# Performance work log

Measured on AMD Instinct MI355X. Metric: run time of the kernel, lower is better.

Reference implementation:

```python
import jax, jax.numpy as jnp
import numpy as np

N_GRAPHS = 512
N_PER_G = 84
N = N_GRAPHS * N_PER_G            # 43008 nodes
E = N_GRAPHS * N_PER_G * N_PER_G  # 3612672 edges (fully connected incl. self-loops)


def setup_inputs() -> dict:
    key = jax.random.key(0)
    ks = jax.random.split(key, 10)
    x = jax.random.normal(ks[0], (N, 84), dtype=jnp.float32)
    # fully-connected edge_index per graph: [2, E], row0=src j, row1=dst i
    off = (np.arange(N_GRAPHS) * N_PER_G)[:, None, None]
    src = (off + np.arange(N_PER_G)[:, None]) + np.zeros((1, 1, N_PER_G), np.int64)
    dst = (off + np.arange(N_PER_G)[None, None, :]) + np.zeros((1, N_PER_G, 1), np.int64)
    edge_index = jnp.asarray(np.stack([src.reshape(-1), dst.reshape(-1)]), dtype=jnp.int64)
    batch = jnp.asarray(np.repeat(np.arange(N_GRAPHS), N_PER_G), dtype=jnp.int64)
    s = 0.1
    W1 = jax.random.normal(ks[1], (84, 64), dtype=jnp.float32) * s
    a_src1 = jax.random.normal(ks[2], (32, 2), dtype=jnp.float32) * s
    a_dst1 = jax.random.normal(ks[3], (32, 2), dtype=jnp.float32) * s
    b1 = jnp.zeros((64,), jnp.float32)
    W2 = jax.random.normal(ks[4], (64, 64), dtype=jnp.float32) * s
    a_src2 = jax.random.normal(ks[5], (1, 64), dtype=jnp.float32) * s
    a_dst2 = jax.random.normal(ks[6], (1, 64), dtype=jnp.float32) * s
    b2 = jnp.zeros((64,), jnp.float32)
    Wfc = jax.random.normal(ks[7], (64, 1), dtype=jnp.float32) * s
    bfc = jnp.zeros((1,), jnp.float32)
    return {"x": x, "edge_index": edge_index, "batch": batch,
            "W1": W1, "a_src1": a_src1, "a_dst1": a_dst1, "b1": b1,
            "W2": W2, "a_src2": a_src2, "a_dst2": a_dst2, "b2": b2,
            "Wfc": Wfc, "bfc": bfc}


def gat_conv(x, W, a_src, a_dst, bias, src, dst, n_heads, ch):
    # x: [N, F] -> h: [N, H, C]
    h = (x @ W).reshape(-1, n_heads, ch)
    alpha_src = jnp.sum(h * a_src, axis=-1)  # [N, H]
    alpha_dst = jnp.sum(h * a_dst, axis=-1)  # [N, H]
    e = jax.nn.leaky_relu(alpha_src[src] + alpha_dst[dst], 0.2)  # [E, H]
    # segment softmax over edges grouped by destination node
    m = jax.ops.segment_max(e, dst, num_segments=N)
    e = jnp.exp(e - m[dst])
    z = jax.ops.segment_sum(e, dst, num_segments=N)
    alpha = e / (z[dst] + 1e-16)                              # [E, H]
    msg = h[src] * alpha[:, :, None]                          # [E, H, C]
    out = jax.ops.segment_sum(msg, dst, num_segments=N)       # [N, H, C]
    return out.reshape(-1, n_heads * ch) + bias


def reference(x, edge_index, batch, W1, a_src1, a_dst1, b1, W2, a_src2, a_dst2, b2, Wfc, bfc):
    src, dst = edge_index[0], edge_index[1]
    h = gat_conv(x, W1, a_src1, a_dst1, b1, src, dst, 32, 2)   # [N, 64]
    h = jax.nn.elu(h)
    h = gat_conv(h, W2, a_src2, a_dst2, b2, src, dst, 1, 64)   # [N, 64]
    # global mean pool per graph
    sums = jax.ops.segment_sum(h, batch, num_segments=N_GRAPHS)
    cnts = jax.ops.segment_sum(jnp.ones((N, 1), h.dtype), batch, num_segments=N_GRAPHS)
    pooled = sums / cnts                                       # [B, 64]
    out = pooled @ Wfc + bfc                                   # [B, 1]
    z = jnp.zeros((1,), jnp.float32)
    return (out, z, z, z, z, z, z)
```

## Files before the change

### kernel.cpp

```cpp
#include <hip/hip_runtime.h>

#define NG 512
#define P  84
#define F0 84
#define F1 64
#define L2E 1.4426950408889634f

#if __has_builtin(__builtin_amdgcn_exp2f)
#define EXP2F(v) __builtin_amdgcn_exp2f(v)
#else
#define EXP2F(v) exp2f(v)
#endif
#if __has_builtin(__builtin_amdgcn_rcpf)
#define RCPF(v) __builtin_amdgcn_rcpf(v)
#else
#define RCPF(v) (1.0f / (v))
#endif


__launch_bounds__(256, 2)
__global__ void gat_fused(const float* __restrict__ x,
                          const float* __restrict__ W1,
                          const float* __restrict__ a_src1,
                          const float* __restrict__ a_dst1,
                          const float* __restrict__ b1,
                          const float* __restrict__ W2,
                          const float* __restrict__ a_src2,
                          const float* __restrict__ a_dst2,
                          const float* __restrict__ b2,
                          const float* __restrict__ Wfc,
                          const float* __restrict__ bfc,
                          float* __restrict__ out)
{
  __shared__ float xs[P * F0];
  __shared__ float wbuf[P * F1];
  __shared__ float h1s[P * F1];
  __shared__ float a2s[2 * F1];
  __shared__ float2 as2p[P];
  __shared__ float2 ad2p[P];
  __shared__ float reds[4 * P];
  __shared__ float redt[P];

  const int tid = threadIdx.x;
  const int ln  = tid & 63;
  const int wid = tid >> 6;
  const int g   = blockIdx.x;
  const int i0  = wid * 21;

  if (g == 0 && tid < 6) out[NG + tid] = 0.f;

  {
    const float4* w4 = (const float4*)W1;
    float4* s4 = (float4*)wbuf;
    #pragma unroll
    for (int t = 0; t < 6; ++t) {
      int idx = tid + t * 256;
      if (idx < (P * F1) / 4) s4[idx] = w4[idx];
    }
    const float4* x4 = (const float4*)(x + (size_t)g * P * F0);
    float4* xs4 = (float4*)xs;
    #pragma unroll
    for (int t = 0; t < 7; ++t) {
      int idx = tid + t * 256;
      if (idx < (P * F0) / 4) xs4[idx] = x4[idx];
    }
    if (tid < F1) a2s[tid] = a_src2[tid] * L2E;
    else if (tid < 2 * F1) a2s[tid] = a_dst2[tid - F1] * L2E;
  }
  __syncthreads();

  {
    float wk[44];
    #pragma unroll
    for (int k = 0; k < 44; ++k) wk[k] = wbuf[k * F1 + ln];
    #pragma unroll 2
    for (int ii = 0; ii < 21; ++ii) {
      const float4* rp = (const float4*)&xs[(i0 + ii) * F0];
      float c0 = 0.f, c1 = 0.f, c2 = 0.f, c3 = 0.f;
      #pragma unroll
      for (int kq = 0; kq < 11; ++kq) {
        float4 v = rp[kq];
        c0 = fmaf(v.x, wk[4 * kq + 0], c0);
        c1 = fmaf(v.y, wk[4 * kq + 1], c1);
        c2 = fmaf(v.z, wk[4 * kq + 2], c2);
        c3 = fmaf(v.w, wk[4 * kq + 3], c3);
      }
      h1s[(i0 + ii) * F1 + ln] = (c0 + c1) + (c2 + c3);
    }
  }
  {
    float wk[40];
    #pragma unroll
    for (int k = 0; k < 40; ++k) wk[k] = wbuf[(44 + k) * F1 + ln];
    #pragma unroll 2
    for (int ii = 0; ii < 21; ++ii) {
      const float4* rp = (const float4*)&xs[(i0 + ii) * F0];
      float c0 = h1s[(i0 + ii) * F1 + ln], c1 = 0.f, c2 = 0.f, c3 = 0.f;
      #pragma unroll
      for (int kq = 0; kq < 10; ++kq) {
        float4 v = rp[11 + kq];
        c0 = fmaf(v.x, wk[4 * kq + 0], c0);
        c1 = fmaf(v.y, wk[4 * kq + 1], c1);
        c2 = fmaf(v.z, wk[4 * kq + 2], c2);
        c3 = fmaf(v.w, wk[4 * kq + 3], c3);
      }
      h1s[(i0 + ii) * F1 + ln] = (c0 + c1) + (c2 + c3);
    }
  }
  __syncthreads();

  {
    float2* pq = (float2*)xs;
    #pragma unroll
    for (int r = 0; r < 11; ++r) {
      int idx = tid + r * 256;
      if (idx < P * 32) {
        int j = idx >> 5, h = idx & 31;
        float2 c = *(const float2*)&h1s[j * F1 + 2 * h];
        float asj = fmaf(c.x, a_src1[2 * h] * L2E, c.y * (a_src1[2 * h + 1] * L2E));
        float2 e; e.x = EXP2F(asj); e.y = EXP2F(0.2f * asj);
        pq[idx] = e;
      }
    }
  }
  const float4* w24 = (const float4*)W2;
  float4 w2r0 = w24[tid];
  float4 w2r1 = w24[tid + 256];
  float4 w2r2 = w24[tid + 512];
  float4 w2r3 = w24[tid + 768];
  __syncthreads();

  {
    const int h  = tid & 31;
    const int ig = tid >> 5;
    const float ada = a_dst1[2 * h] * L2E, adb = a_dst1[2 * h + 1] * L2E;
    float pi[11], qi[11], sm[11], m0[11], m1[11];
    #pragma unroll
    for (int t = 0; t < 11; ++t) {
      int i = ig + 8 * t; int ie = i < P ? i : P - 1;
      float2 c = *(const float2*)&h1s[ie * F1 + 2 * h];
      float adi = fmaf(c.x, ada, c.y * adb);
      pi[t] = EXP2F(adi); qi[t] = EXP2F(0.2f * adi);
      sm[t] = 0.f; m0[t] = 0.f; m1[t] = 0.f;
    }
    const float2* pq = (const float2*)xs;
    #pragma unroll 2
    for (int j = 0; j < P; ++j) {
      float2 c = *(const float2*)&h1s[j * F1 + 2 * h];
      float2 e = pq[j * 32 + h];
      #pragma unroll
      for (int t = 0; t < 11; ++t) {
        float p = fmaxf(e.x * pi[t], e.y * qi[t]);
        sm[t] += p;
        m0[t] = fmaf(p, c.x, m0[t]);
        m1[t] = fmaf(p, c.y, m1[t]);
      }
    }
    const float bc0 = b1[2 * h], bc1 = b1[2 * h + 1];
    float* o1 = wbuf;
    #pragma unroll
    for (int t = 0; t < 11; ++t) {
      int i = ig + 8 * t;
      if (i < P) {
        float rz = RCPF(sm[t]);
        float u0 = fmaf(m0[t], rz, bc0);
        float u1 = fmaf(m1[t], rz, bc1);
        u0 = u0 > 0.f ? u0 : (__expf(u0) - 1.f);
        u1 = u1 > 0.f ? u1 : (__expf(u1) - 1.f);
        float2 oo; oo.x = u0; oo.y = u1;
        *(float2*)&o1[i * F1 + 2 * h] = oo;
      }
    }
  }
  __syncthreads();

  {
    float4* s4 = (float4*)xs;
    s4[tid]       = w2r0;
    s4[tid + 256] = w2r1;
    s4[tid + 512] = w2r2;
    s4[tid + 768] = w2r3;
  }
  __syncthreads();

  {
    float wk[32];
    #pragma unroll
    for (int k = 0; k < 32; ++k) wk[k] = xs[k * F1 + ln];
    #pragma unroll 2
    for (int ii = 0; ii < 21; ++ii) {
      const float4* rp = (const float4*)&wbuf[(i0 + ii) * F1];
      float c0 = 0.f, c1 = 0.f, c2 = 0.f, c3 = 0.f;
      #pragma unroll
      for (int kq = 0; kq < 8; ++kq) {
        float4 v = rp[kq];
        c0 = fmaf(v.x, wk[4 * kq + 0], c0);
        c1 = fmaf(v.y, wk[4 * kq + 1], c1);
        c2 = fmaf(v.z, wk[4 * kq + 2], c2);
        c3 = fmaf(v.w, wk[4 * kq + 3], c3);
      }
      h1s[(i0 + ii) * F1 + ln] = (c0 + c1) + (c2 + c3);
    }
  }
  {
    float wk[32];
    #pragma unroll
    for (int k = 0; k < 32; ++k) wk[k] = xs[(32 + k) * F1 + ln];
    #pragma unroll 2
    for (int ii = 0; ii < 21; ++ii) {
      const float4* rp = (const float4*)&wbuf[(i0 + ii) * F1];
      float c0 = h1s[(i0 + ii) * F1 + ln], c1 = 0.f, c2 = 0.f, c3 = 0.f;
      #pragma unroll
      for (int kq = 0; kq < 8; ++kq) {
        float4 v = rp[8 + kq];
        c0 = fmaf(v.x, wk[4 * kq + 0], c0);
        c1 = fmaf(v.y, wk[4 * kq + 1], c1);
        c2 = fmaf(v.z, wk[4 * kq + 2], c2);
        c3 = fmaf(v.w, wk[4 * kq + 3], c3);
      }
      h1s[(i0 + ii) * F1 + ln] = (c0 + c1) + (c2 + c3);
    }
  }
  __syncthreads();

  if (tid < P) {
    float s = 0.f, d = 0.f;
    #pragma unroll 4
    for (int f = 0; f < F1; ++f) {
      int fp = (f + tid) & 63;
      float c = h1s[tid * F1 + fp];
      s = fmaf(c, a2s[fp], s);
      d = fmaf(c, a2s[F1 + fp], d);
    }
    float2 ps; ps.x = EXP2F(s); ps.y = EXP2F(0.2f * s);
    float2 pd; pd.x = EXP2F(d); pd.y = EXP2F(0.2f * d);
    as2p[tid] = ps; ad2p[tid] = pd;
  }
  __syncthreads();

  {
    const float2 S0 = as2p[ln];
    float2 S1; S1.x = 0.f; S1.y = 0.f;
    if (ln < P - 64) S1 = as2p[64 + ln];
    float sj0 = 0.f, sj1 = 0.f;
    for (int ii = 0; ii < 21; ++ii) {
      float2 D = ad2p[i0 + ii];
      float p0 = fmaxf(S0.x * D.x, S0.y * D.y);
      float p1 = (ln < P - 64) ? fmaxf(S1.x * D.x, S1.y * D.y) : 0.f;
      float ss = p0 + p1;
      #pragma unroll
      for (int off = 32; off > 0; off >>= 1) ss += __shfl_xor(ss, off, 64);
      float rz = RCPF(ss);
      sj0 = fmaf(p0, rz, sj0);
      sj1 = fmaf(p1, rz, sj1);
    }
    reds[wid * P + ln] = sj0;
    if (ln < P - 64) reds[wid * P + 64 + ln] = sj1;
  }
  __syncthreads();

  if (tid < P) {
    float s = 0.f;
    #pragma unroll
    for (int w = 0; w < 4; ++w) s += reds[w * P + tid];
    redt[tid] = s;
  }
  __syncthreads();

  if (wid == 0) {
    float c0 = 0.f, c1 = 0.f, c2 = 0.f, c3 = 0.f;
    for (int j = 0; j < P; j += 4) {
      c0 = fmaf(redt[j],     h1s[(j + 0) * F1 + ln], c0);
      c1 = fmaf(redt[j + 1], h1s[(j + 1) * F1 + ln], c1);
      c2 = fmaf(redt[j + 2], h1s[(j + 2) * F1 + ln], c2);
      c3 = fmaf(redt[j + 3], h1s[(j + 3) * F1 + ln], c3);
    }
    float pooled = ((c0 + c1) + (c2 + c3)) * (1.f / 84.f) + b2[ln];
    float v = pooled * Wfc[ln];
    #pragma unroll
    for (int off = 32; off > 0; off >>= 1) v += __shfl_xor(v, off, 64);
    if (ln == 0) out[g] = v + bfc[0];
  }
}

extern "C" void kernel_launch(void* const* d_in, const int* in_sizes, int n_in,
                              void* d_out, int out_size, void* d_ws, size_t ws_size,
                              hipStream_t stream) {
  const float* x      = (const float*)d_in[0];
  const float* W1     = (const float*)d_in[3];
  const float* a_src1 = (const float*)d_in[4];
  const float* a_dst1 = (const float*)d_in[5];
  const float* b1     = (const float*)d_in[6];
  const float* W2     = (const float*)d_in[7];
  const float* a_src2 = (const float*)d_in[8];
  const float* a_dst2 = (const float*)d_in[9];
  const float* b2     = (const float*)d_in[10];
  const float* Wfc    = (const float*)d_in[11];
  const float* bfc    = (const float*)d_in[12];
  hipLaunchKernelGGL(gat_fused, dim3(NG), dim3(256), 0, stream,
                     x, W1, a_src1, a_dst1, b1, W2, a_src2, a_dst2, b2, Wfc, bfc,
                     (float*)d_out);
}
```

Measured before the change: 153.5 us.

## Read x rows directly from global, shrink LDS, split attention dot across lanes

Drops the shared-memory staging of the per-graph x tile. The first GEMM now reads x rows straight from global memory using a wave-uniform offset (readfirstlane), so the loads can become scalar or broadcast. The pq/W2 scratch gets its own smaller buffer, cutting LDS usage, which may allow higher occupancy, and W2 is staged with float2 loads. The layer-2 attention-score dot product is split across two lanes per node and combined with a shuffle. The cost is more global-memory traffic in the GEMM, relying on cache hits for the repeated row reads.

```diff
diff --git a/kernel.cpp b/kernel.cpp
--- a/kernel.cpp
+++ b/kernel.cpp
@@ -32,14 +32,14 @@
                           const float* __restrict__ bfc,
                           float* __restrict__ out)
 {
-  __shared__ float xs[P * F0];
-  __shared__ float wbuf[P * F1];
-  __shared__ float h1s[P * F1];
-  __shared__ float a2s[2 * F1];
+  __shared__ float  wbuf[P * F1];
+  __shared__ float  h1s[P * F1];
+  __shared__ float2 pqs[P * 32];
+  __shared__ float  a2s[2 * F1];
   __shared__ float2 as2p[P];
   __shared__ float2 ad2p[P];
-  __shared__ float reds[4 * P];
-  __shared__ float redt[P];
+  __shared__ float  reds[4 * P];
+  __shared__ float  redt[P];
 
   const int tid = threadIdx.x;
   const int ln  = tid & 63;
@@ -49,6 +49,8 @@
 
   if (g == 0 && tid < 6) out[NG + tid] = 0.f;
 
+  const float* xg = x + (size_t)g * P * F0;
+
   {
     const float4* w4 = (const float4*)W1;
     float4* s4 = (float4*)wbuf;
@@ -57,13 +59,6 @@
       int idx = tid + t * 256;
       if (idx < (P * F1) / 4) s4[idx] = w4[idx];
     }
-    const float4* x4 = (const float4*)(x + (size_t)g * P * F0);
-    float4* xs4 = (float4*)xs;
-    #pragma unroll
-    for (int t = 0; t < 7; ++t) {
-      int idx = tid + t * 256;
-      if (idx < (P * F0) / 4) xs4[idx] = x4[idx];
-    }
     if (tid < F1) a2s[tid] = a_src2[tid] * L2E;
     else if (tid < 2 * F1) a2s[tid] = a_dst2[tid - F1] * L2E;
   }
@@ -75,7 +70,8 @@
     for (int k = 0; k < 44; ++k) wk[k] = wbuf[k * F1 + ln];
     #pragma unroll 2
     for (int ii = 0; ii < 21; ++ii) {
-      const float4* rp = (const float4*)&xs[(i0 + ii) * F0];
+      const int roff = __builtin_amdgcn_readfirstlane((i0 + ii) * F0);
+      const float4* rp = (const float4*)(xg + roff);
       float c0 = 0.f, c1 = 0.f, c2 = 0.f, c3 = 0.f;
       #pragma unroll
       for (int kq = 0; kq < 11; ++kq) {
@@ -94,7 +90,8 @@
     for (int k = 0; k < 40; ++k) wk[k] = wbuf[(44 + k) * F1 + ln];
     #pragma unroll 2
     for (int ii = 0; ii < 21; ++ii) {
-      const float4* rp = (const float4*)&xs[(i0 + ii) * F0];
+      const int roff = __builtin_amdgcn_readfirstlane((i0 + ii) * F0);
+      const float4* rp = (const float4*)(xg + roff);
       float c0 = h1s[(i0 + ii) * F1 + ln], c1 = 0.f, c2 = 0.f, c3 = 0.f;
       #pragma unroll
       for (int kq = 0; kq < 10; ++kq) {
@@ -110,7 +107,6 @@
   __syncthreads();
 
   {
-    float2* pq = (float2*)xs;
     #pragma unroll
     for (int r = 0; r < 11; ++r) {
       int idx = tid + r * 256;
@@ -119,15 +115,14 @@
         float2 c = *(const float2*)&h1s[j * F1 + 2 * h];
         float asj = fmaf(c.x, a_src1[2 * h] * L2E, c.y * (a_src1[2 * h + 1] * L2E));
         float2 e; e.x = EXP2F(asj); e.y = EXP2F(0.2f * asj);
-        pq[idx] = e;
-      }
-    }
-  }
-  const float4* w24 = (const float4*)W2;
-  float4 w2r0 = w24[tid];
-  float4 w2r1 = w24[tid + 256];
-  float4 w2r2 = w24[tid + 512];
-  float4 w2r3 = w24[tid + 768];
+        pqs[idx] = e;
+      }
+    }
+  }
+  const float2* w22 = (const float2*)W2;
+  float2 w2r[8];
+  #pragma unroll
+  for (int t = 0; t < 8; ++t) w2r[t] = w22[tid + t * 256];
   __syncthreads();
 
   {
@@ -143,11 +138,10 @@
       pi[t] = EXP2F(adi); qi[t] = EXP2F(0.2f * adi);
       sm[t] = 0.f; m0[t] = 0.f; m1[t] = 0.f;
     }
-    const float2* pq = (const float2*)xs;
     #pragma unroll 2
     for (int j = 0; j < P; ++j) {
       float2 c = *(const float2*)&h1s[j * F1 + 2 * h];
-      float2 e = pq[j * 32 + h];
+      float2 e = pqs[j * 32 + h];
       #pragma unroll
       for (int t = 0; t < 11; ++t) {
         float p = fmaxf(e.x * pi[t], e.y * qi[t]);
@@ -175,18 +169,17 @@
   __syncthreads();
 
   {
-    float4* s4 = (float4*)xs;
-    s4[tid]       = w2r0;
-    s4[tid + 256] = w2r1;
-    s4[tid + 512] = w2r2;
-    s4[tid + 768] = w2r3;
-  }
-  __syncthreads();
-
-  {
+    float2* s2 = (float2*)pqs;
+    #pragma unroll
+    for (int t = 0; t < 8; ++t) s2[tid + t * 256] = w2r[t];
+  }
+  __syncthreads();
+
+  {
+    const float* w2s = (const float*)pqs;
     float wk[32];
     #pragma unroll
-    for (int k = 0; k < 32; ++k) wk[k] = xs[k * F1 + ln];
+    for (int k = 0; k < 32; ++k) wk[k] = w2s[k * F1 + ln];
     #pragma unroll 2
     for (int ii = 0; ii < 21; ++ii) {
       const float4* rp = (const float4*)&wbuf[(i0 + ii) * F1];
@@ -203,9 +196,10 @@
     }
   }
   {
+    const float* w2s = (const float*)pqs;
     float wk[32];
     #pragma unroll
-    for (int k = 0; k < 32; ++k) wk[k] = xs[(32 + k) * F1 + ln];
+    for (int k = 0; k < 32; ++k) wk[k] = w2s[(32 + k) * F1 + ln];
     #pragma unroll 2
     for (int ii = 0; ii < 21; ++ii) {
       const float4* rp = (const float4*)&wbuf[(i0 + ii) * F1];
@@ -223,18 +217,23 @@
   }
   __syncthreads();
 
-  if (tid < P) {
+  if (tid < 2 * P) {
+    const int n = tid >> 1, q = tid & 1;
     float s = 0.f, d = 0.f;
-    #pragma unroll 4
-    for (int f = 0; f < F1; ++f) {
-      int fp = (f + tid) & 63;
-      float c = h1s[tid * F1 + fp];
-      s = fmaf(c, a2s[fp], s);
-      d = fmaf(c, a2s[F1 + fp], d);
-    }
-    float2 ps; ps.x = EXP2F(s); ps.y = EXP2F(0.2f * s);
-    float2 pd; pd.x = EXP2F(d); pd.y = EXP2F(0.2f * d);
-    as2p[tid] = ps; ad2p[tid] = pd;
+    #pragma unroll 8
+    for (int t = 0; t < 32; ++t) {
+      int f = q * 32 + ((t + n) & 31);
+      float c = h1s[n * F1 + f];
+      s = fmaf(c, a2s[f], s);
+      d = fmaf(c, a2s[F1 + f], d);
+    }
+    s += __shfl_xor(s, 1, 64);
+    d += __shfl_xor(d, 1, 64);
+    if (q == 0) {
+      float2 ps; ps.x = EXP2F(s); ps.y = EXP2F(0.2f * s);
+      float2 pd; pd.x = EXP2F(d); pd.y = EXP2F(0.2f * d);
+      as2p[n] = ps; ad2p[n] = pd;
+    }
   }
   __syncthreads();
 
```

After: 169.8 us. +10.6%, slower.
